# Kernel optimization log

Hardware: AMD Instinct MI355X
Metric: run time of the kernel (lower is better)

Reference implementation:

```python
import jax, jax.numpy as jnp
import numpy as np

DIM = 768
HEADS = 12
HEAD_DIM = DIM // HEADS
SCALE = HEAD_DIM ** -0.5
B = 8
N = 2121   # 1 cls + 1600 + 400 + 100 + 20 text
NT = 20

# token ranges: cls [0,1), x0 [1,1601), x1 [1601,2001), x2 [2001,2101), t [2101,2121)
SLICES = {'cls': (0, 1), 'x0': (1, 1601), 'x1': (1601, 2001), 'x2': (2001, 2101), 't': (2101, 2121)}


def setup_inputs() -> dict:
    key = jax.random.key(0)
    k1, k2, k3, k4 = jax.random.split(key, 4)
    src = jax.random.normal(k1, (B, N, DIM), dtype=jnp.float32)
    visu_mask = jnp.zeros((B, 2101), dtype=bool)   # True = masked out
    text_mask = jnp.zeros((B, NT), dtype=bool)
    w_qkv = jax.random.normal(k2, (DIM, 3 * DIM), dtype=jnp.float32) * 0.02
    w_proj = jax.random.normal(k3, (DIM, DIM), dtype=jnp.float32) * 0.02
    b_proj = jax.random.normal(k4, (DIM,), dtype=jnp.float32) * 0.02
    return {'src': src, 'visu_mask': visu_mask, 'text_mask': text_mask,
            'w_qkv': w_qkv, 'w_proj': w_proj, 'b_proj': b_proj}


def _attn(q, k, v, mask):
    # q: [B,H,Nq,D], k/v: [B,H,Nk,D], mask: [B,Nk] bool (True = masked)
    scores = jnp.einsum('bhqd,bhkd->bhqk', q * SCALE, k)
    scores = jnp.where(mask[:, None, None, :], -jnp.inf, scores)
    p = jax.nn.softmax(scores, axis=-1)
    o = jnp.einsum('bhqk,bhkd->bhqd', p, v)          # [B,H,Nq,D]
    return o.transpose(0, 2, 1, 3).reshape(q.shape[0], q.shape[2], -1)  # [B,Nq,C]


def reference(src, visu_mask, text_mask, w_qkv, w_proj, b_proj):
    qkv = (src @ w_qkv).reshape(B, N, 3, HEADS, HEAD_DIM).transpose(2, 0, 3, 1, 4)
    q, k, v = qkv[0], qkv[1], qkv[2]                  # [B,H,N,D]

    def blk(t, lo, hi):
        return t[:, :, lo:hi, :]

    (c0, c1), (a0, a1), (b0, b1), (d0, d1), (t0, t1) = (
        SLICES['cls'], SLICES['x0'], SLICES['x1'], SLICES['x2'], SLICES['t'])

    x0_mask = visu_mask[:, a0:a1]
    x1_mask = visu_mask[:, b0:b1]
    x2_mask = visu_mask[:, d0:d1]
    full_mask = jnp.concatenate([visu_mask, text_mask], axis=1)   # [B, N]

    # cls attends to everything
    cls = _attn(blk(q, c0, c1), k, v, full_mask)
    # x2 attends to x0+x1+x2+t
    k_x2 = jnp.concatenate([blk(k, a0, a1), blk(k, b0, b1), blk(k, d0, d1), blk(k, t0, t1)], axis=2)
    v_x2 = jnp.concatenate([blk(v, a0, a1), blk(v, b0, b1), blk(v, d0, d1), blk(v, t0, t1)], axis=2)
    m_x2 = jnp.concatenate([x0_mask, x1_mask, x2_mask, text_mask], axis=1)
    x2 = _attn(blk(q, d0, d1), k_x2, v_x2, m_x2)
    # x1 attends to x0+x1+t
    k_x1 = jnp.concatenate([blk(k, a0, a1), blk(k, b0, b1), blk(k, t0, t1)], axis=2)
    v_x1 = jnp.concatenate([blk(v, a0, a1), blk(v, b0, b1), blk(v, t0, t1)], axis=2)
    m_x1 = jnp.concatenate([x0_mask, x1_mask, text_mask], axis=1)
    x1 = _attn(blk(q, b0, b1), k_x1, v_x1, m_x1)
    # x0 attends to x0+t
    k_x0 = jnp.concatenate([blk(k, a0, a1), blk(k, t0, t1)], axis=2)
    v_x0 = jnp.concatenate([blk(v, a0, a1), blk(v, t0, t1)], axis=2)
    m_x0 = jnp.concatenate([x0_mask, text_mask], axis=1)
    x0 = _attn(blk(q, a0, a1), k_x0, v_x0, m_x0)
    # text attends to everything
    t = _attn(blk(q, t0, t1), k, v, full_mask)

    x = jnp.concatenate([cls, x0, x1, x2, t], axis=1)
    return x @ w_proj + b_proj
```

## Files before the change

kernel.cpp:

```cpp
#include <hip/hip_runtime.h>
#include <stdint.h>

typedef short           bf16x8 __attribute__((ext_vector_type(8)));
typedef float           f32x4  __attribute__((ext_vector_type(4)));
typedef float           f32x16 __attribute__((ext_vector_type(16)));
typedef unsigned short  u16;
typedef u16             u16x8  __attribute__((ext_vector_type(8)));
typedef uint32_t        u32;
typedef unsigned long long u64;

#define NB    8
#define NSEQ  2121
#define NPAD  2176
#define MROWS 16968
#define MPAD  17024
#define NH    12

#if __has_builtin(__builtin_amdgcn_exp2f)
#define EXP2F(x) __builtin_amdgcn_exp2f(x)
#else
#define EXP2F(x) exp2f(x)
#endif

#define INVALID_S   (-90000.0f)

__device__ __forceinline__ u16 f2bf(float f) {
  uint32_t u = __float_as_uint(f);
  u += 0x7fffu + ((u >> 16) & 1u);
  return (u16)(u >> 16);
}

__device__ __forceinline__ void gld_lds16(const void* g, void* l) {
  __builtin_amdgcn_global_load_lds(
      (const __attribute__((address_space(1))) unsigned int*)g,
      (__attribute__((address_space(3))) unsigned int*)l, 16, 0, 0);
}

__global__ void transpose_cast(const float* __restrict__ in, u16* __restrict__ out,
                               int R, int C, int scale_cols, float scale)
{
  __shared__ float tile[32][33];
  const int c0 = blockIdx.x * 32, r0 = blockIdx.y * 32;
  const int tx = threadIdx.x, ty = threadIdx.y;
#pragma unroll
  for (int i = 0; i < 4; i++) {
    const int r = r0 + ty + i * 8;
    tile[ty + i * 8][tx] = in[(size_t)r * C + c0 + tx];
  }
  __syncthreads();
#pragma unroll
  for (int i = 0; i < 4; i++) {
    const int c = c0 + ty + i * 8;
    float v = tile[tx][ty + i * 8];
    if (c < scale_cols) v *= scale;
    out[(size_t)c * R + r0 + tx] = f2bf(v);
  }
}

__global__ __launch_bounds__(256) void cast_src_bf16(const float* __restrict__ in,
                                                     u16* __restrict__ out)
{
  const size_t i = ((size_t)blockIdx.x * 256 + threadIdx.x) * 8;
  float4 a = *(const float4*)(in + i);
  float4 b = *(const float4*)(in + i + 4);
  u16x8 t;
  t[0] = f2bf(a.x); t[1] = f2bf(a.y); t[2] = f2bf(a.z); t[3] = f2bf(a.w);
  t[4] = f2bf(b.x); t[5] = f2bf(b.y); t[6] = f2bf(b.z); t[7] = f2bf(b.w);
  *(u16x8*)(out + i) = t;
}

__global__ __launch_bounds__(256) void gemm_qkv_kernel(
    const u16* __restrict__ srcb, const u16* __restrict__ wt,
    u16* __restrict__ qk, u16* __restrict__ vt)
{
  __shared__ u16 Asf[2][128 * 32];
  __shared__ u16 Bsf[2][128 * 32];
  const int tid  = threadIdx.x;
  const int lane = tid & 63, wave = tid >> 6;
  const int wr = wave >> 1, wc = wave & 1;
  const int col = lane & 15, grp = lane >> 4;
  const int m0 = blockIdx.y * 128, n0 = blockIdx.x * 128;

  const f32x4 fz = {0.f, 0.f, 0.f, 0.f};
  f32x4 acc[4][4];
#pragma unroll
  for (int i = 0; i < 4; i++)
#pragma unroll
    for (int j = 0; j < 4; j++) acc[i][j] = fz;

  const int arow = tid >> 2, akoff = (tid & 3) * 8;
  const u16* ag = srcb + (size_t)(m0 + arow) * 768 + akoff;
  const u16* bg = wt   + (size_t)(n0 + arow) * 768 + akoff;
  const int lofs = wave * 512;

  gld_lds16(ag,                    &Asf[0][lofs]);
  gld_lds16(ag + (size_t)64 * 768, &Asf[0][lofs + 2048]);
  gld_lds16(bg,                    &Bsf[0][lofs]);
  gld_lds16(bg + (size_t)64 * 768, &Bsf[0][lofs + 2048]);

  int cur = 0;
  for (int kb = 0; kb < 768; kb += 32) {
    __syncthreads();
    if (kb + 32 < 768) {
      gld_lds16(ag + kb + 32,                    &Asf[cur ^ 1][lofs]);
      gld_lds16(ag + kb + 32 + (size_t)64 * 768, &Asf[cur ^ 1][lofs + 2048]);
      gld_lds16(bg + kb + 32,                    &Bsf[cur ^ 1][lofs]);
      gld_lds16(bg + kb + 32 + (size_t)64 * 768, &Bsf[cur ^ 1][lofs + 2048]);
    }

    bf16x8 af[4], bfr[4];
#pragma unroll
    for (int mt = 0; mt < 4; mt++) af[mt]  = *(const bf16x8*)&Asf[cur][(wr * 64 + mt * 16 + col) * 32 + grp * 8];
#pragma unroll
    for (int nt = 0; nt < 4; nt++) bfr[nt] = *(const bf16x8*)&Bsf[cur][(wc * 64 + nt * 16 + col) * 32 + grp * 8];
#pragma unroll
    for (int mt = 0; mt < 4; mt++)
#pragma unroll
      for (int nt = 0; nt < 4; nt++)
        acc[mt][nt] = __builtin_amdgcn_mfma_f32_16x16x32_bf16(af[mt], bfr[nt], acc[mt][nt], 0, 0, 0);
    cur ^= 1;
  }

#pragma unroll
  for (int mt = 0; mt < 4; mt++) {
#pragma unroll
    for (int r = 0; r < 4; r++) {
      const int mm = m0 + wr * 64 + mt * 16 + grp * 4 + r;
      if (mm >= MROWS) continue;
      const uint32_t bb = (uint32_t)mm / 2121u;
      const uint32_t nn = (uint32_t)mm - bb * 2121u;
#pragma unroll
      for (int nt = 0; nt < 4; nt++) {
        const int c = n0 + wc * 64 + nt * 16 + col;
        const u16 bits = f2bf(acc[mt][nt][r]);
        if (c < 1536) {
          qk[(size_t)mm * 1536 + c] = bits;
        } else {
          const int hd = c - 1536;
          const int h = hd >> 6, d = hd & 63;
          vt[((size_t)(bb * NH + h) * 64 + d) * NPAD + nn] = bits;
        }
      }
    }
  }
}

__global__ __launch_bounds__(256) void gemm_proj_kernel(
    const u16* __restrict__ A, const u16* __restrict__ Bt,
    const float* __restrict__ bias, float* __restrict__ out)
{
  __shared__ u16 Asf[2][128 * 32];
  __shared__ u16 Bsf[2][128 * 32];
  const int tid  = threadIdx.x;
  const int lane = tid & 63, wave = tid >> 6;
  const int wr = wave >> 1, wc = wave & 1;
  const int col = lane & 15, grp = lane >> 4;
  const int m0 = blockIdx.y * 128, n0 = blockIdx.x * 128;

  const f32x4 fz = {0.f, 0.f, 0.f, 0.f};
  f32x4 acc[4][4];
#pragma unroll
  for (int i = 0; i < 4; i++)
#pragma unroll
    for (int j = 0; j < 4; j++) acc[i][j] = fz;

  const int arow = tid >> 2, akoff = (tid & 3) * 8;
  const u16* ag = A  + (size_t)(m0 + arow) * 768 + akoff;
  const u16* bg = Bt + (size_t)(n0 + arow) * 768 + akoff;
  const int lofs = wave * 512;

  gld_lds16(ag,                    &Asf[0][lofs]);
  gld_lds16(ag + (size_t)64 * 768, &Asf[0][lofs + 2048]);
  gld_lds16(bg,                    &Bsf[0][lofs]);
  gld_lds16(bg + (size_t)64 * 768, &Bsf[0][lofs + 2048]);

  int cur = 0;
  for (int kb = 0; kb < 768; kb += 32) {
    __syncthreads();
    if (kb + 32 < 768) {
      gld_lds16(ag + kb + 32,                    &Asf[cur ^ 1][lofs]);
      gld_lds16(ag + kb + 32 + (size_t)64 * 768, &Asf[cur ^ 1][lofs + 2048]);
      gld_lds16(bg + kb + 32,                    &Bsf[cur ^ 1][lofs]);
      gld_lds16(bg + kb + 32 + (size_t)64 * 768, &Bsf[cur ^ 1][lofs + 2048]);
    }

    bf16x8 af[4], bfr[4];
#pragma unroll
    for (int mt = 0; mt < 4; mt++) af[mt]  = *(const bf16x8*)&Asf[cur][(wr * 64 + mt * 16 + col) * 32 + grp * 8];
#pragma unroll
    for (int nt = 0; nt < 4; nt++) bfr[nt] = *(const bf16x8*)&Bsf[cur][(wc * 64 + nt * 16 + col) * 32 + grp * 8];
#pragma unroll
    for (int mt = 0; mt < 4; mt++)
#pragma unroll
      for (int nt = 0; nt < 4; nt++)
        acc[mt][nt] = __builtin_amdgcn_mfma_f32_16x16x32_bf16(af[mt], bfr[nt], acc[mt][nt], 0, 0, 0);
    cur ^= 1;
  }

#pragma unroll
  for (int mt = 0; mt < 4; mt++) {
#pragma unroll
    for (int r = 0; r < 4; r++) {
      const int mm = m0 + wr * 64 + mt * 16 + grp * 4 + r;
      if (mm >= MROWS) continue;
#pragma unroll
      for (int nt = 0; nt < 4; nt++) {
        const int c = n0 + wc * 64 + nt * 16 + col;
        out[(size_t)mm * 768 + c] = acc[mt][nt][r] + bias[c];
      }
    }
  }
}

__global__ __launch_bounds__(512) void attn_kernel(
    const u16* __restrict__ qkbuf, const u16* __restrict__ vt,
    const unsigned char* __restrict__ visu, const unsigned char* __restrict__ text,
    u16* __restrict__ attnout)
{
  __shared__ __align__(16) u16 Ks[2][64][72];
  __shared__ __align__(16) u16 Vs[2][64][72];
  __shared__ __align__(16) u64 mb64[34];
  __shared__ __align__(16) float lduf[8][32];

  const int tid  = threadIdx.x;
  const int lane = tid & 63, wave = tid >> 6;
  const int l31 = lane & 31, h = lane >> 5;

  const int fid = blockIdx.x;
  const int swz = (fid & 7) * 108 + (fid >> 3);
  const int qtile = swz % 9;
  const int bh = swz / 9;
  const int b = bh / NH, hh = bh % NH;
  const int qt0 = qtile * 256;
  const int q0 = qt0 + wave * 32;
  const int qrow = q0 + l31;

  for (int c = wave; c < 34; c += 8) {
    const int key = c * 64 + lane;
    int mb = 1;
    if (key < 2101)      mb = visu[b * 2101 + key] ? 1 : 0;
    else if (key < 2121) mb = text[b * 20 + (key - 2101)] ? 1 : 0;
    const u64 bal = __ballot(mb != 0);
    if (lane == 0) mb64[c] = bal;
  }

  const int qload = (qrow < NSEQ) ? qrow : (NSEQ - 1);
  bf16x8 qf[4];
  {
    const u16* qp = qkbuf + (size_t)(b * NSEQ + qload) * 1536 + hh * 64 + h * 8;
#pragma unroll
    for (int s = 0; s < 4; s++) qf[s] = *(const bf16x8*)(qp + s * 16);
  }

  int ks, ke, ex;
  if (qrow == 0)        { ks = 0; ke = 2121; ex = 0; }
  else if (qrow < 1601) { ks = 1; ke = 1601; ex = 1; }
  else if (qrow < 2001) { ks = 1; ke = 2001; ex = 1; }
  else if (qrow < 2101) { ks = 1; ke = 2121; ex = 0; }
  else if (qrow < 2121) { ks = 0; ke = 2121; ex = 0; }
  else                  { ks = 0; ke = 0;    ex = 0; }

  const int hi = (qt0 + 255 < 2120) ? (qt0 + 255) : 2120;
  int ke_tile, extra;
  if (qt0 == 0 || hi >= 2001) { ke_tile = 2121; extra = 0; }
  else if (hi >= 1601)        { ke_tile = 2001; extra = 1; }
  else                        { ke_tile = 1601; extra = 1; }
  const int nkv = (ke_tile + 63) >> 6;
  const int ntot = nkv + extra;

  f32x16 O0, O1;
#pragma unroll
  for (int i = 0; i < 16; i++) { O0[i] = 0.f; O1[i] = 0.f; }
  float lrun = 0.f;

  const int srow = tid >> 3, skoff = (tid & 7) * 8;
  const size_t vbase = (size_t)(b * NH + hh) * 64 * NPAD;
  const u16* kbase = qkbuf + (size_t)(b * NSEQ + srow) * 1536 + 768 + hh * 64 + skoff;
  const u16* vrow  = vt + vbase + (size_t)srow * NPAD + skoff;

  *(u16x8*)&Ks[0][srow][skoff] = *(const u16x8*)kbase;
  *(u16x8*)&Vs[0][srow][skoff] = *(const u16x8*)vrow;
  __syncthreads();

  u16x8 kpre, vpre;

  for (int it = 0; it < ntot; ++it) {
    const int cur = it & 1;
    const int kv0 = (it < nkv) ? it * 64 : 2096;
    const bool more = (it + 1 < ntot);

    if (more) {
      const int kvn = (it + 1 < nkv) ? (it + 1) * 64 : 2096;
      kpre = *(const u16x8*)(kbase + (size_t)kvn * 1536);
      vpre = *(const u16x8*)(vrow + kvn);
    }

    const int skipl = (kv0 >= ke) && !((ex != 0) && (kv0 < 2121) && (kv0 + 64 > 2101));
    if (!__all(skipl)) {
      f32x16 S0, S1;
#pragma unroll
      for (int i = 0; i < 16; i++) { S0[i] = 0.f; S1[i] = 0.f; }
      __builtin_amdgcn_s_setprio(1);
#pragma unroll
      for (int s = 0; s < 4; s++) {
        const bf16x8 k0 = *(const bf16x8*)&Ks[cur][l31][s * 16 + h * 8];
        const bf16x8 k1 = *(const bf16x8*)&Ks[cur][32 + l31][s * 16 + h * 8];
        S0 = __builtin_amdgcn_mfma_f32_32x32x16_bf16(k0, qf[s], S0, 0, 0, 0);
        S1 = __builtin_amdgcn_mfma_f32_32x32x16_bf16(k1, qf[s], S1, 0, 0, 0);
      }
      __builtin_amdgcn_s_setprio(0);

      const int fastl = (kv0 >= ks) && (kv0 + 64 <= ke);
      const u64 mword = (it < nkv) ? mb64[it] : ((mb64[32] >> 48) | (mb64[33] << 16));
      const bool plain = __all(fastl) && (mword == 0ull);
      if (!plain) {
        const u32 wlo = (u32)mword, whi = (u32)(mword >> 32);
#pragma unroll
        for (int m = 0; m < 4; m++) {
#pragma unroll
          for (int r = 0; r < 4; r++) {
            const int bitpos = 8 * m + 4 * h + r;
            {
              const int key = kv0 + bitpos;
              bool valid = ((key >= ks) && (key < ke)) || ((ex != 0) && (key >= 2101));
              valid = valid && (((wlo >> bitpos) & 1u) == 0u);
              S0[4 * m + r] = valid ? S0[4 * m + r] : INVALID_S;
            }
            {
              const int key = kv0 + 32 + bitpos;
              bool valid = ((key >= ks) && (key < ke)) || ((ex != 0) && (key >= 2101));
              valid = valid && (((whi >> bitpos) & 1u) == 0u);
              S1[4 * m + r] = valid ? S1[4 * m + r] : INVALID_S;
            }
          }
        }
      }

      float ls = 0.f;
#pragma unroll
      for (int i = 0; i < 16; i++) { const float p = EXP2F(S0[i]); S0[i] = p; ls += p; }
#pragma unroll
      for (int i = 0; i < 16; i++) { const float p = EXP2F(S1[i]); S1[i] = p; ls += p; }
      lrun += ls;

      bf16x8 pa[4];
      {
        u32 w[8];
#pragma unroll
        for (int j = 0; j < 8; j++) {
          u32 t;
          asm("v_cvt_pk_bf16_f32 %0, %1, %2" : "=v"(t) : "v"(S0[2 * j]), "v"(S0[2 * j + 1]));
          w[j] = t;
        }
        asm("v_permlane32_swap_b32 %0, %1" : "+v"(w[0]), "+v"(w[2]));
        asm("v_permlane32_swap_b32 %0, %1" : "+v"(w[1]), "+v"(w[3]));
        asm("v_permlane32_swap_b32 %0, %1" : "+v"(w[4]), "+v"(w[6]));
        asm("v_permlane32_swap_b32 %0, %1" : "+v"(w[5]), "+v"(w[7]));
        union { u32 u[4]; bf16x8 v; } f0, f1;
        f0.u[0] = w[0]; f0.u[1] = w[1]; f0.u[2] = w[2]; f0.u[3] = w[3];
        f1.u[0] = w[4]; f1.u[1] = w[5]; f1.u[2] = w[6]; f1.u[3] = w[7];
        pa[0] = f0.v; pa[1] = f1.v;
      }
      {
        u32 w[8];
#pragma unroll
        for (int j = 0; j < 8; j++) {
          u32 t;
          asm("v_cvt_pk_bf16_f32 %0, %1, %2" : "=v"(t) : "v"(S1[2 * j]), "v"(S1[2 * j + 1]));
          w[j] = t;
        }
        asm("v_permlane32_swap_b32 %0, %1" : "+v"(w[0]), "+v"(w[2]));
        asm("v_permlane32_swap_b32 %0, %1" : "+v"(w[1]), "+v"(w[3]));
        asm("v_permlane32_swap_b32 %0, %1" : "+v"(w[4]), "+v"(w[6]));
        asm("v_permlane32_swap_b32 %0, %1" : "+v"(w[5]), "+v"(w[7]));
        union { u32 u[4]; bf16x8 v; } f0, f1;
        f0.u[0] = w[0]; f0.u[1] = w[1]; f0.u[2] = w[2]; f0.u[3] = w[3];
        f1.u[0] = w[4]; f1.u[1] = w[5]; f1.u[2] = w[6]; f1.u[3] = w[7];
        pa[2] = f0.v; pa[3] = f1.v;
      }

      __builtin_amdgcn_s_setprio(1);
#pragma unroll
      for (int ck = 0; ck < 4; ck++) {
        const bf16x8 vf0 = *(const bf16x8*)&Vs[cur][l31][ck * 16 + h * 8];
        const bf16x8 vf1 = *(const bf16x8*)&Vs[cur][32 + l31][ck * 16 + h * 8];
        O0 = __builtin_amdgcn_mfma_f32_32x32x16_bf16(pa[ck], vf0, O0, 0, 0, 0);
        O1 = __builtin_amdgcn_mfma_f32_32x32x16_bf16(pa[ck], vf1, O1, 0, 0, 0);
      }
      __builtin_amdgcn_s_setprio(0);
    }

    if (more) {
      *(u16x8*)&Ks[cur ^ 1][srow][skoff] = kpre;
      *(u16x8*)&Vs[cur ^ 1][srow][skoff] = vpre;
    }
    __syncthreads();
  }

  float ltot = lrun + __shfl_xor(lrun, 32);
  if (h == 0) lduf[wave][l31] = ltot;
#pragma unroll
  for (int m = 0; m < 4; m++) {
    const f32x4 lv = *(const f32x4*)&lduf[wave][8 * m + 4 * h];
#pragma unroll
    for (int r = 0; r < 4; r++) {
      const float linv = (lv[r] > 0.f) ? 1.0f / lv[r] : 0.f;
      const int n = q0 + 8 * m + 4 * h + r;
      if (n >= NSEQ) continue;
      u16* op = attnout + (size_t)(b * NSEQ + n) * 768 + hh * 64 + l31;
      op[0]  = f2bf(O0[4 * m + r] * linv);
      op[32] = f2bf(O1[4 * m + r] * linv);
    }
  }
}

extern "C" void kernel_launch(void* const* d_in, const int* in_sizes, int n_in,
                              void* d_out, int out_size, void* d_ws, size_t ws_size,
                              hipStream_t stream) {
  const float* src  = (const float*)d_in[0];
  const unsigned char* visu = (const unsigned char*)d_in[1];
  const unsigned char* text = (const unsigned char*)d_in[2];
  const float* w_qkv = (const float*)d_in[3];
  const float* w_proj = (const float*)d_in[4];
  const float* b_proj = (const float*)d_in[5];
  float* out = (float*)d_out;

  char* ws = (char*)d_ws;
  size_t off = 0;
  auto alloc = [&](size_t bytes) { char* p = ws + off; off += (bytes + 255) & ~(size_t)255; return p; };
  u16* wqkv_t  = (u16*)alloc((size_t)2304 * 768 * 2);
  u16* wproj_t = (u16*)alloc((size_t)768 * 768 * 2);
  u16* qk      = (u16*)alloc((size_t)MPAD * 1536 * 2);
  u16* vtb     = (u16*)alloc((size_t)NB * NH * 64 * NPAD * 2);
  u16* tmp0    = (u16*)alloc((size_t)MPAD * 768 * 2);
  (void)ws_size; (void)in_sizes; (void)n_in; (void)out_size;

  transpose_cast<<<dim3(2304 / 32, 768 / 32), dim3(32, 8), 0, stream>>>(w_qkv, wqkv_t, 768, 2304, 768, 0.125f * 1.4426950408889634f);
  transpose_cast<<<dim3(768 / 32, 768 / 32), dim3(32, 8), 0, stream>>>(w_proj, wproj_t, 768, 768, 0, 1.0f);
  cast_src_bf16<<<dim3(6363), dim3(256), 0, stream>>>(src, tmp0);
  gemm_qkv_kernel<<<dim3(18, 133), dim3(256), 0, stream>>>(tmp0, wqkv_t, qk, vtb);
  attn_kernel<<<dim3(864), dim3(512), 0, stream>>>(qk, vtb, visu, text, tmp0);
  gemm_proj_kernel<<<dim3(6, 133), dim3(256), 0, stream>>>(tmp0, wproj_t, b_proj, out);
}
```

Baseline: 371.3 us.

## Stage 128-key K/V tiles per barrier in attention loop

The attention kernel now loads two 64-key K/V sub-tiles into double-buffered shared memory per iteration and processes them in an inner loop. This halves the number of __syncthreads barriers and global-to-LDS staging rounds per query tile, and each thread issues wider prefetch loads. In exchange it roughly doubles shared-memory use per block, which can reduce occupancy, and adds prefetch registers. Special handling keeps the single trailing text-key tile at offset 2096.

After: 362.2 us. 1.03x faster.

```diff
diff --git a/kernel.cpp b/kernel.cpp
--- a/kernel.cpp
+++ b/kernel.cpp
@@ -217,8 +217,8 @@
     const unsigned char* __restrict__ visu, const unsigned char* __restrict__ text,
     u16* __restrict__ attnout)
 {
-  __shared__ __align__(16) u16 Ks[2][64][72];
-  __shared__ __align__(16) u16 Vs[2][64][72];
+  __shared__ __align__(16) u16 Ks[2][128][72];
+  __shared__ __align__(16) u16 Vs[2][64][136];
   __shared__ __align__(16) u64 mb64[34];
   __shared__ __align__(16) float lduf[8][32];
 
@@ -266,52 +266,74 @@
   else if (hi >= 1601)        { ke_tile = 2001; extra = 1; }
   else                        { ke_tile = 1601; extra = 1; }
   const int nkv = (ke_tile + 63) >> 6;
-  const int ntot = nkv + extra;
+  const int npair = nkv >> 1;
+  const int ntotp = npair + extra;
 
   f32x16 O0, O1;
 #pragma unroll
   for (int i = 0; i < 16; i++) { O0[i] = 0.f; O1[i] = 0.f; }
   float lrun = 0.f;
 
-  const int srow = tid >> 3, skoff = (tid & 7) * 8;
+  const int srow = tid >> 2, skoff = (tid & 3) * 16;
+  const int vd = tid >> 3, vkoff = (tid & 7) * 16;
   const size_t vbase = (size_t)(b * NH + hh) * 64 * NPAD;
   const u16* kbase = qkbuf + (size_t)(b * NSEQ + srow) * 1536 + 768 + hh * 64 + skoff;
-  const u16* vrow  = vt + vbase + (size_t)srow * NPAD + skoff;
-
-  *(u16x8*)&Ks[0][srow][skoff] = *(const u16x8*)kbase;
-  *(u16x8*)&Vs[0][srow][skoff] = *(const u16x8*)vrow;
+  const u16* vsrc  = vt + vbase + (size_t)vd * NPAD + vkoff;
+
+  {
+    *(u16x8*)&Ks[0][srow][skoff]     = *(const u16x8*)kbase;
+    *(u16x8*)&Ks[0][srow][skoff + 8] = *(const u16x8*)(kbase + 8);
+    *(u16x8*)&Vs[0][vd][vkoff]       = *(const u16x8*)vsrc;
+    *(u16x8*)&Vs[0][vd][vkoff + 8]   = *(const u16x8*)(vsrc + 8);
+  }
   __syncthreads();
 
-  u16x8 kpre, vpre;
-
-  for (int it = 0; it < ntot; ++it) {
+  u16x8 kpreA = {0,0,0,0,0,0,0,0}, kpreB = kpreA, vpreA = kpreA, vpreB = kpreA;
+
+  for (int it = 0; it < ntotp; ++it) {
     const int cur = it & 1;
-    const int kv0 = (it < nkv) ? it * 64 : 2096;
-    const bool more = (it + 1 < ntot);
+    const bool isPair = it < npair;
+    const int kvbase = isPair ? it * 128 : 2096;
+    const bool more = (it + 1 < ntotp);
+    const bool nextPair = (it + 1 < npair);
 
     if (more) {
-      const int kvn = (it + 1 < nkv) ? (it + 1) * 64 : 2096;
-      kpre = *(const u16x8*)(kbase + (size_t)kvn * 1536);
-      vpre = *(const u16x8*)(vrow + kvn);
-    }
-
-    const int skipl = (kv0 >= ke) && !((ex != 0) && (kv0 < 2121) && (kv0 + 64 > 2101));
-    if (!__all(skipl)) {
+      const int nb = nextPair ? (it + 1) * 128 : 2096;
+      if (nextPair || srow < 64) {
+        const u16* kp = kbase + (size_t)nb * 1536;
+        kpreA = *(const u16x8*)kp;
+        kpreB = *(const u16x8*)(kp + 8);
+      }
+      if (nextPair || vkoff < 64) {
+        const u16* vp = vsrc + nb;
+        vpreA = *(const u16x8*)vp;
+        vpreB = *(const u16x8*)(vp + 8);
+      }
+    }
+
+    const int nsub = isPair ? 2 : 1;
+    for (int sub = 0; sub < nsub; ++sub) {
+      const int kv0 = kvbase + sub * 64;
+      const int soff = sub * 64;
+
+      const int skipl = (kv0 >= ke) && !((ex != 0) && (kv0 < 2121) && (kv0 + 64 > 2101));
+      if (__all(skipl)) continue;
+
       f32x16 S0, S1;
 #pragma unroll
       for (int i = 0; i < 16; i++) { S0[i] = 0.f; S1[i] = 0.f; }
       __builtin_amdgcn_s_setprio(1);
 #pragma unroll
       for (int s = 0; s < 4; s++) {
-        const bf16x8 k0 = *(const bf16x8*)&Ks[cur][l31][s * 16 + h * 8];
-        const bf16x8 k1 = *(const bf16x8*)&Ks[cur][32 + l31][s * 16 + h * 8];
+        const bf16x8 k0 = *(const bf16x8*)&Ks[cur][soff + l31][s * 16 + h * 8];
+        const bf16x8 k1 = *(const bf16x8*)&Ks[cur][soff + 32 + l31][s * 16 + h * 8];
         S0 = __builtin_amdgcn_mfma_f32_32x32x16_bf16(k0, qf[s], S0, 0, 0, 0);
         S1 = __builtin_amdgcn_mfma_f32_32x32x16_bf16(k1, qf[s], S1, 0, 0, 0);
       }
       __builtin_amdgcn_s_setprio(0);
 
       const int fastl = (kv0 >= ks) && (kv0 + 64 <= ke);
-      const u64 mword = (it < nkv) ? mb64[it] : ((mb64[32] >> 48) | (mb64[33] << 16));
+      const u64 mword = isPair ? mb64[it * 2 + sub] : ((mb64[32] >> 48) | (mb64[33] << 16));
       const bool plain = __all(fastl) && (mword == 0ull);
       if (!plain) {
         const u32 wlo = (u32)mword, whi = (u32)(mword >> 32);
@@ -382,8 +404,8 @@
       __builtin_amdgcn_s_setprio(1);
 #pragma unroll
       for (int ck = 0; ck < 4; ck++) {
-        const bf16x8 vf0 = *(const bf16x8*)&Vs[cur][l31][ck * 16 + h * 8];
-        const bf16x8 vf1 = *(const bf16x8*)&Vs[cur][32 + l31][ck * 16 + h * 8];
+        const bf16x8 vf0 = *(const bf16x8*)&Vs[cur][l31][soff + ck * 16 + h * 8];
+        const bf16x8 vf1 = *(const bf16x8*)&Vs[cur][32 + l31][soff + ck * 16 + h * 8];
         O0 = __builtin_amdgcn_mfma_f32_32x32x16_bf16(pa[ck], vf0, O0, 0, 0, 0);
         O1 = __builtin_amdgcn_mfma_f32_32x32x16_bf16(pa[ck], vf1, O1, 0, 0, 0);
       }
@@ -391,8 +413,14 @@
     }
 
     if (more) {
-      *(u16x8*)&Ks[cur ^ 1][srow][skoff] = kpre;
-      *(u16x8*)&Vs[cur ^ 1][srow][skoff] = vpre;
+      if (nextPair || srow < 64) {
+        *(u16x8*)&Ks[cur ^ 1][srow][skoff]     = kpreA;
+        *(u16x8*)&Ks[cur ^ 1][srow][skoff + 8] = kpreB;
+      }
+      if (nextPair || vkoff < 64) {
+        *(u16x8*)&Vs[cur ^ 1][vd][vkoff]       = vpreA;
+        *(u16x8*)&Vs[cur ^ 1][vd][vkoff + 8]   = vpreB;
+      }
     }
     __syncthreads();
   }
```
